# Kernel tuning notes

Measured on AMD Instinct MI355X. Metric: run time of the kernel, lower is better.

Reference implementation:

```python
import jax, jax.numpy as jnp
import numpy as np
import math

D_MODEL = 1024
N_HEADS = 16
HEAD_DIM = D_MODEL // N_HEADS
SEQ_LEN = 8192
INCLUDE_LOCAL = 2


def get_dilated_positions(seq_len, include_local=2):
    # Faithful numpy port of the torch pattern generator (runs once at setup).
    max_attend = include_local + int(math.ceil(math.log2(seq_len + 1)))
    positions = np.zeros((seq_len, max_attend), dtype=np.int64)
    mask = np.zeros((seq_len, max_attend), dtype=bool)
    for i in range(seq_len):
        ap = [i]
        for j in range(1, include_local + 1):
            if i - j >= 0:
                ap.append(i - j)
        k = 2
        while i - 2 ** k >= 0:
            ap.append(i - 2 ** k)
            k += 1
        positions[i, :len(ap)] = ap
        mask[i, :len(ap)] = True
    return positions, mask


def setup_inputs() -> dict:
    key = jax.random.key(0)
    kx, kq, kk, kv, ko = jax.random.split(key, 5)
    x = jax.random.normal(kx, (1, SEQ_LEN, D_MODEL), dtype=jnp.float32)
    # nn.Linear(bias=False) weights, torch layout [out_features, in_features]
    s = 0.02
    q_w = jax.random.normal(kq, (D_MODEL, D_MODEL), dtype=jnp.float32) * s
    k_w = jax.random.normal(kk, (D_MODEL, D_MODEL), dtype=jnp.float32) * s
    v_w = jax.random.normal(kv, (D_MODEL, D_MODEL), dtype=jnp.float32) * s
    o_w = jax.random.normal(ko, (D_MODEL, D_MODEL), dtype=jnp.float32) * s
    pos_np, mask_np = get_dilated_positions(SEQ_LEN, INCLUDE_LOCAL)
    return {
        "x": x,
        "q_w": q_w, "k_w": k_w, "v_w": v_w, "o_w": o_w,
        "positions": jnp.asarray(pos_np),   # (S, A) int64 indices
        "attend_mask": jnp.asarray(mask_np) # (S, A) bool
    }


def reference(x, q_w, k_w, v_w, o_w, positions, attend_mask):
    B, S, _ = x.shape
    H, Dh = N_HEADS, HEAD_DIM
    scale = Dh ** -0.5

    q = (x @ q_w.T).reshape(B, S, H, Dh).transpose(0, 2, 1, 3)  # (B,H,S,Dh)
    k = (x @ k_w.T).reshape(B, S, H, Dh).transpose(0, 2, 1, 3)
    v = (x @ v_w.T).reshape(B, S, H, Dh).transpose(0, 2, 1, 3)

    # Gather K/V at the dilated positions: (B,H,S,A,Dh)
    k_sparse = k[:, :, positions, :]
    v_sparse = v[:, :, positions, :]

    scores = jnp.einsum('bhsd,bhsad->bhsa', q, k_sparse) * scale
    scores = jnp.where(attend_mask[None, None, :, :], scores, -jnp.inf)
    attn = jax.nn.softmax(scores, axis=-1)  # dropout p in eval / 0.0 -> identity

    out = jnp.einsum('bhsa,bhsad->bhsd', attn, v_sparse)
    out = out.transpose(0, 2, 1, 3).reshape(B, S, D_MODEL)
    return out @ o_w.T
```

## Files before the change

### kernel.cpp

```cpp
#include <hip/hip_runtime.h>
#include <hip/hip_bf16.h>

typedef __bf16 bf16_t;
typedef __bf16 bf16x4 __attribute__((ext_vector_type(4)));
typedef __bf16 bf16x8 __attribute__((ext_vector_type(8)));
typedef float floatx16 __attribute__((ext_vector_type(16)));

#define SEQ    8192
#define DM     1024
#define NHEADS 16
#define HDIM   64

__device__ __forceinline__ void async_ld16(bf16_t* lds, const bf16_t* g) {
  __builtin_amdgcn_global_load_lds(
      (__attribute__((address_space(1))) void*)g,
      (__attribute__((address_space(3))) void*)lds, 16, 0, 0);
}

__global__ __launch_bounds__(256)
void cvt_all(const float* __restrict__ x,  const float* __restrict__ qw,
             const float* __restrict__ kw, const float* __restrict__ vw,
             const float* __restrict__ ow,
             bf16_t* __restrict__ Xb,  bf16_t* __restrict__ QWb,
             bf16_t* __restrict__ KWb, bf16_t* __restrict__ VWb,
             bf16_t* __restrict__ OWb) {
  const int b = blockIdx.x;
  const float* in; bf16_t* out; int g;
  if (b < 8192) { in = x; out = Xb; g = b; }
  else {
    const int w  = (b - 8192) >> 10;
    const int wb = (b - 8192) & 1023;
    switch (w) {
      case 0:  in = qw; out = QWb; break;
      case 1:  in = kw; out = KWb; break;
      case 2:  in = vw; out = VWb; break;
      default: in = ow; out = OWb; break;
    }
    g = wb;
  }
  const int idx = (g * 256 + threadIdx.x) * 4;
  float4 v = *(const float4*)(in + idx);
  bf16x4 o = { (bf16_t)v.x, (bf16_t)v.y, (bf16_t)v.z, (bf16_t)v.w };
  *(bf16x4*)(out + idx) = o;
}

__global__ __launch_bounds__(256)
void gemm_qkv(const bf16_t* __restrict__ A,
              const bf16_t* __restrict__ Bq, const bf16_t* __restrict__ Bk,
              const bf16_t* __restrict__ Bv,
              bf16_t* __restrict__ Cq, bf16_t* __restrict__ Ck, bf16_t* __restrict__ Cv)
{
  const bf16_t* B = (blockIdx.z == 0) ? Bq : (blockIdx.z == 1) ? Bk : Bv;
  bf16_t*       C = (blockIdx.z == 0) ? Cq : (blockIdx.z == 1) ? Ck : Cv;
  constexpr int Kdim = DM;
  __shared__ __attribute__((aligned(16))) bf16_t sA[128 * 64];
  __shared__ __attribute__((aligned(16))) bf16_t sB[128 * 64];

  const int tid  = threadIdx.x;
  const int wave = tid >> 6;
  const int lane = tid & 63;
  const int l31  = lane & 31;
  const int half = lane >> 5;
  const int wr   = (wave >> 1) * 64;
  const int wc   = (wave & 1) * 64;

  const int gc = (lane & 7) ^ ((lane >> 3) & 7);
  const size_t arow0 = (size_t)blockIdx.x * 128 + wave * 32 + (lane >> 3);
  const size_t brow0 = (size_t)blockIdx.y * 128 + wave * 32 + (lane >> 3);
  const bf16_t* Ag = A + arow0 * Kdim + gc * 8;
  const bf16_t* Bg = B + brow0 * Kdim + gc * 8;
  bf16_t* sAw = sA + wave * 32 * 64;
  bf16_t* sBw = sB + wave * 32 * 64;

  floatx16 acc[2][2];
  #pragma unroll
  for (int i = 0; i < 2; ++i)
    #pragma unroll
    for (int j = 0; j < 2; ++j)
      acc[i][j] = (floatx16)(0.0f);

  const int sw = l31 & 7;

  for (int ko = 0; ko < Kdim; ko += 64) {
    #pragma unroll
    for (int n = 0; n < 4; ++n) {
      async_ld16(sAw + n * 512, Ag + (size_t)n * 8 * Kdim + ko);
      async_ld16(sBw + n * 512, Bg + (size_t)n * 8 * Kdim + ko);
    }
    __syncthreads();

    #pragma unroll
    for (int s = 0; s < 4; ++s) {
      const int ck   = s * 2 + half;
      const int slot = (ck ^ sw) * 8;
      bf16x8 af[2], bfr[2];
      #pragma unroll
      for (int mi = 0; mi < 2; ++mi)
        af[mi] = *(const bf16x8*)&sA[(wr + mi * 32 + l31) * 64 + slot];
      #pragma unroll
      for (int ni = 0; ni < 2; ++ni)
        bfr[ni] = *(const bf16x8*)&sB[(wc + ni * 32 + l31) * 64 + slot];

      #pragma unroll
      for (int mi = 0; mi < 2; ++mi)
        #pragma unroll
        for (int ni = 0; ni < 2; ++ni)
          acc[mi][ni] = __builtin_amdgcn_mfma_f32_32x32x16_bf16(af[mi], bfr[ni], acc[mi][ni], 0, 0, 0);
    }

    __syncthreads();
  }

  const float scl = (blockIdx.z == 0) ? 0.125f : 1.0f;
  const int crow0 = blockIdx.x * 128 + wr + 4 * half;
  const int ccol0 = blockIdx.y * 128 + wc + l31;
  #pragma unroll
  for (int mi = 0; mi < 2; ++mi)
    #pragma unroll
    for (int ni = 0; ni < 2; ++ni)
      #pragma unroll
      for (int r = 0; r < 16; ++r) {
        const int row = crow0 + mi * 32 + (r & 3) + 8 * (r >> 2);
        C[(size_t)row * DM + (ccol0 + ni * 32)] = (bf16_t)(acc[mi][ni][r] * scl);
      }
}

__global__ __launch_bounds__(256)
void gemm_out(const bf16_t* __restrict__ A, const bf16_t* __restrict__ B,
              float* __restrict__ C)
{
  constexpr int Kdim = DM;
  __shared__ __attribute__((aligned(16))) bf16_t sA[128 * 32];
  __shared__ __attribute__((aligned(16))) bf16_t sB[64 * 32];

  const int tid  = threadIdx.x;
  const int wave = tid >> 6;
  const int lane = tid & 63;
  const int l31  = lane & 31;
  const int half = lane >> 5;
  const int wr   = (wave >> 1) * 64;
  const int wc   = (wave & 1) * 32;

  const int gc = (lane & 3) ^ ((lane >> 3) & 3);
  const size_t arow = (size_t)blockIdx.x * 128 + wave * 32 + (lane >> 2);
  const size_t brow = (size_t)blockIdx.y * 64 + wave * 16 + (lane >> 2);
  const bf16_t* Ag = A + arow * Kdim + gc * 8;
  const bf16_t* Bg = B + brow * Kdim + gc * 8;
  bf16_t* sAw = sA + wave * 32 * 32;
  bf16_t* sBw = sB + wave * 16 * 32;

  floatx16 acc[2];
  acc[0] = (floatx16)(0.0f);
  acc[1] = (floatx16)(0.0f);

  const int sw = (l31 >> 1) & 3;

  for (int ko = 0; ko < Kdim; ko += 32) {
    async_ld16(sAw,           Ag + ko);
    async_ld16(sAw + 16 * 32, Ag + 16 * Kdim + ko);
    async_ld16(sBw,           Bg + ko);
    __syncthreads();

    #pragma unroll
    for (int s = 0; s < 2; ++s) {
      const int ck   = s * 2 + half;
      const int slot = (ck ^ sw) * 8;
      bf16x8 af[2], bfr;
      #pragma unroll
      for (int mi = 0; mi < 2; ++mi)
        af[mi] = *(const bf16x8*)&sA[(wr + mi * 32 + l31) * 32 + slot];
      bfr = *(const bf16x8*)&sB[(wc + l31) * 32 + slot];

      #pragma unroll
      for (int mi = 0; mi < 2; ++mi)
        acc[mi] = __builtin_amdgcn_mfma_f32_32x32x16_bf16(af[mi], bfr, acc[mi], 0, 0, 0);
    }

    __syncthreads();
  }

  const int crow0 = blockIdx.x * 128 + wr + 4 * half;
  const int ccol  = blockIdx.y * 64 + wc + l31;
  #pragma unroll
  for (int mi = 0; mi < 2; ++mi)
    #pragma unroll
    for (int r = 0; r < 16; ++r) {
      const int row = crow0 + mi * 32 + (r & 3) + 8 * (r >> 2);
      C[(size_t)row * DM + ccol] = acc[mi][r];
    }
}

__global__ __launch_bounds__(256)
void dilated_attn(const bf16_t* __restrict__ Q, const bf16_t* __restrict__ K,
                  const bf16_t* __restrict__ V, bf16_t* O)
{
  __shared__ float sM[2][64];
  __shared__ float sL[2][64];
  __shared__ float sAcc[2][64][17];

  const int lane = threadIdx.x & 63;
  const int wv   = threadIdx.x >> 6;
  const int ql   = wv >> 1;
  const int sub  = wv & 1;
  const int qb   = (blockIdx.x & 7) * 512 + (blockIdx.x >> 3);
  const int i    = qb * 2 + ql;
  const size_t base = (size_t)i * DM + lane * 16;

  bf16x8 q0 = *(const bf16x8*)(Q + base);
  bf16x8 q1 = *(const bf16x8*)(Q + base + 8);
  float qf[16];
  #pragma unroll
  for (int j = 0; j < 8; ++j) { qf[j] = (float)q0[j]; qf[j + 8] = (float)q1[j]; }

  const int npos = (i == 0) ? 1 : (33 - __builtin_clz((unsigned)i));
  auto pos_addr = [&](int t) -> size_t {
    const int off = (t == 0) ? 0 : (1 << (t - 1));
    return (size_t)(i - off) * DM + lane * 16;
  };

  float m = -INFINITY, l = 0.0f;
  float acc[16];
  #pragma unroll
  for (int j = 0; j < 16; ++j) acc[j] = 0.0f;

  int t = sub;
  if (t < npos) {
    size_t a = pos_addr(t);
    bf16x8 k0 = *(const bf16x8*)(K + a), k1 = *(const bf16x8*)(K + a + 8);
    bf16x8 v0 = *(const bf16x8*)(V + a), v1 = *(const bf16x8*)(V + a + 8);
    while (true) {
      const int tn = t + 2;
      const bool more = (tn < npos);
      bf16x8 nk0, nk1, nv0, nv1;
      if (more) {
        const size_t na = pos_addr(tn);
        nk0 = *(const bf16x8*)(K + na); nk1 = *(const bf16x8*)(K + na + 8);
        nv0 = *(const bf16x8*)(V + na); nv1 = *(const bf16x8*)(V + na + 8);
      }

      float sc = 0.0f;
      #pragma unroll
      for (int j = 0; j < 8; ++j) sc += qf[j] * (float)k0[j] + qf[j + 8] * (float)k1[j];
      sc += __shfl_xor(sc, 1, 64);
      sc += __shfl_xor(sc, 2, 64);

      float mn = fmaxf(m, sc);
      float co = __expf(m - mn);
      float w  = __expf(sc - mn);
      l = l * co + w;
      m = mn;
      #pragma unroll
      for (int j = 0; j < 8; ++j) {
        acc[j]     = acc[j]     * co + w * (float)v0[j];
        acc[j + 8] = acc[j + 8] * co + w * (float)v1[j];
      }

      if (!more) break;
      k0 = nk0; k1 = nk1; v0 = nv0; v1 = nv1;
      t = tn;
    }
  }

  if (sub == 1) {
    sM[ql][lane] = m;
    sL[ql][lane] = l;
    #pragma unroll
    for (int j = 0; j < 16; ++j) sAcc[ql][lane][j] = acc[j];
  }
  __syncthreads();
  if (sub == 0) {
    const float mb = sM[ql][lane], lb = sL[ql][lane];
    const float mt = fmaxf(m, mb);
    const float ca = __expf(m - mt);
    const float cb = __expf(mb - mt);
    const float inv = 1.0f / (l * ca + lb * cb);
    bf16x8 o0, o1;
    #pragma unroll
    for (int j = 0; j < 8; ++j) {
      o0[j] = (bf16_t)((acc[j]     * ca + sAcc[ql][lane][j]     * cb) * inv);
      o1[j] = (bf16_t)((acc[j + 8] * ca + sAcc[ql][lane][j + 8] * cb) * inv);
    }
    *(bf16x8*)(O + base)     = o0;
    *(bf16x8*)(O + base + 8) = o1;
  }
}

extern "C" void kernel_launch(void* const* d_in, const int* in_sizes, int n_in,
                              void* d_out, int out_size, void* d_ws, size_t ws_size,
                              hipStream_t stream) {
  (void)in_sizes; (void)n_in; (void)out_size; (void)ws_size;
  const float* x  = (const float*)d_in[0];
  const float* qw = (const float*)d_in[1];
  const float* kw = (const float*)d_in[2];
  const float* vw = (const float*)d_in[3];
  const float* ow = (const float*)d_in[4];
  float* out = (float*)d_out;

  bf16_t* Xb  = (bf16_t*)d_ws;
  bf16_t* Qb  = Xb  + (size_t)SEQ * DM;
  bf16_t* Kb  = Qb  + (size_t)SEQ * DM;
  bf16_t* Vb  = Kb  + (size_t)SEQ * DM;
  bf16_t* QWb = Vb  + (size_t)SEQ * DM;
  bf16_t* KWb = QWb + (size_t)DM * DM;
  bf16_t* VWb = KWb + (size_t)DM * DM;
  bf16_t* OWb = VWb + (size_t)DM * DM;
  bf16_t* AO  = Qb;

  cvt_all<<<dim3(8192 + 4096), dim3(256), 0, stream>>>(x, qw, kw, vw, ow,
                                                       Xb, QWb, KWb, VWb, OWb);

  dim3 block(256);
  gemm_qkv<<<dim3(SEQ / 128, DM / 128, 3), block, 0, stream>>>(Xb, QWb, KWb, VWb, Qb, Kb, Vb);
  dilated_attn<<<dim3(SEQ / 2), block, 0, stream>>>(Qb, Kb, Vb, AO);
  gemm_out<<<dim3(SEQ / 128, DM / 64), block, 0, stream>>>(AO, OWb, out);
}
```

Before: 215.9 us.

## Unify GEMMs into double-buffered 256x128 tile core with 8 waves

Replaces the QKV and output GEMMs with one shared templated core that uses 256x128 tiles, 512 threads (8 waves) and double-buffered LDS. Global-to-LDS async loads for the next K tile are spread across the MFMA substeps, with barriers and raised wave priority around the MFMA groups. The goal is to hide load latency, overlap memory with compute, and cut per-tile barrier overhead and block count. In exchange it uses more LDS per block (96 KB), which may limit occupancy, and the output GEMM now launches fewer, larger blocks.

```diff
diff --git a/kernel.cpp b/kernel.cpp
--- a/kernel.cpp
+++ b/kernel.cpp
@@ -44,33 +44,29 @@
   *(bf16x4*)(out + idx) = o;
 }
 
-__global__ __launch_bounds__(256)
-void gemm_qkv(const bf16_t* __restrict__ A,
-              const bf16_t* __restrict__ Bq, const bf16_t* __restrict__ Bk,
-              const bf16_t* __restrict__ Bv,
-              bf16_t* __restrict__ Cq, bf16_t* __restrict__ Ck, bf16_t* __restrict__ Cv)
-{
-  const bf16_t* B = (blockIdx.z == 0) ? Bq : (blockIdx.z == 1) ? Bk : Bv;
-  bf16_t*       C = (blockIdx.z == 0) ? Cq : (blockIdx.z == 1) ? Ck : Cv;
+template <typename OutT>
+__device__ __forceinline__ void gemm_core_256x128(
+    const bf16_t* __restrict__ A, const bf16_t* __restrict__ B,
+    OutT* __restrict__ C, float scl)
+{
   constexpr int Kdim = DM;
-  __shared__ __attribute__((aligned(16))) bf16_t sA[128 * 64];
-  __shared__ __attribute__((aligned(16))) bf16_t sB[128 * 64];
+  constexpr int NT   = Kdim / 64;
+  __shared__ __attribute__((aligned(16))) bf16_t sA[2][256 * 64];
+  __shared__ __attribute__((aligned(16))) bf16_t sB[2][128 * 64];
 
   const int tid  = threadIdx.x;
   const int wave = tid >> 6;
   const int lane = tid & 63;
   const int l31  = lane & 31;
   const int half = lane >> 5;
-  const int wr   = (wave >> 1) * 64;
-  const int wc   = (wave & 1) * 64;
+  const int wm   = wave >> 1;
+  const int wn   = wave & 1;
 
   const int gc = (lane & 7) ^ ((lane >> 3) & 7);
-  const size_t arow0 = (size_t)blockIdx.x * 128 + wave * 32 + (lane >> 3);
-  const size_t brow0 = (size_t)blockIdx.y * 128 + wave * 32 + (lane >> 3);
-  const bf16_t* Ag = A + arow0 * Kdim + gc * 8;
-  const bf16_t* Bg = B + brow0 * Kdim + gc * 8;
-  bf16_t* sAw = sA + wave * 32 * 64;
-  bf16_t* sBw = sB + wave * 32 * 64;
+  const size_t arow = (size_t)blockIdx.x * 256 + wave * 8 + (lane >> 3);
+  const size_t brow = (size_t)blockIdx.y * 128 + wave * 8 + (lane >> 3);
+  const bf16_t* Ag = A + arow * Kdim + gc * 8;
+  const bf16_t* Bg = B + brow * Kdim + gc * 8;
 
   floatx16 acc[2][2];
   #pragma unroll
@@ -79,41 +75,58 @@
     for (int j = 0; j < 2; ++j)
       acc[i][j] = (floatx16)(0.0f);
 
+  #pragma unroll
+  for (int j = 0; j < 4; ++j)
+    async_ld16(&sA[0][(j * 64 + wave * 8) * 64], Ag + (size_t)j * 64 * Kdim);
+  #pragma unroll
+  for (int j = 0; j < 2; ++j)
+    async_ld16(&sB[0][(j * 64 + wave * 8) * 64], Bg + (size_t)j * 64 * Kdim);
+  __syncthreads();
+
   const int sw = l31 & 7;
 
-  for (int ko = 0; ko < Kdim; ko += 64) {
-    #pragma unroll
-    for (int n = 0; n < 4; ++n) {
-      async_ld16(sAw + n * 512, Ag + (size_t)n * 8 * Kdim + ko);
-      async_ld16(sBw + n * 512, Bg + (size_t)n * 8 * Kdim + ko);
-    }
+  for (int kt = 0; kt < NT; ++kt) {
+    const int  cur = kt & 1;
+    const int  nxt = cur ^ 1;
+    const int  ko  = (kt + 1) * 64;
+    const bool pre = (kt + 1 < NT);
+
+    #pragma unroll
+    for (int s = 0; s < 4; ++s) {
+      const int slot = ((s * 2 + half) ^ sw) * 8;
+      bf16x8 af0 = *(const bf16x8*)&sA[cur][(wm * 64      + l31) * 64 + slot];
+      bf16x8 af1 = *(const bf16x8*)&sA[cur][(wm * 64 + 32 + l31) * 64 + slot];
+      bf16x8 bf0 = *(const bf16x8*)&sB[cur][(wn * 64      + l31) * 64 + slot];
+      bf16x8 bf1 = *(const bf16x8*)&sB[cur][(wn * 64 + 32 + l31) * 64 + slot];
+
+      if (pre) {
+        if (s == 0) {
+          async_ld16(&sA[nxt][(0 * 64 + wave * 8) * 64], Ag + (size_t)0 * 64 * Kdim + ko);
+          async_ld16(&sA[nxt][(1 * 64 + wave * 8) * 64], Ag + (size_t)1 * 64 * Kdim + ko);
+        } else if (s == 1) {
+          async_ld16(&sA[nxt][(2 * 64 + wave * 8) * 64], Ag + (size_t)2 * 64 * Kdim + ko);
+          async_ld16(&sA[nxt][(3 * 64 + wave * 8) * 64], Ag + (size_t)3 * 64 * Kdim + ko);
+        } else if (s == 2) {
+          async_ld16(&sB[nxt][(0 * 64 + wave * 8) * 64], Bg + ko);
+          async_ld16(&sB[nxt][(1 * 64 + wave * 8) * 64], Bg + (size_t)64 * Kdim + ko);
+        }
+      }
+
+      __builtin_amdgcn_s_barrier();
+      __builtin_amdgcn_s_setprio(1);
+      acc[0][0] = __builtin_amdgcn_mfma_f32_32x32x16_bf16(af0, bf0, acc[0][0], 0, 0, 0);
+      acc[0][1] = __builtin_amdgcn_mfma_f32_32x32x16_bf16(af0, bf1, acc[0][1], 0, 0, 0);
+      acc[1][0] = __builtin_amdgcn_mfma_f32_32x32x16_bf16(af1, bf0, acc[1][0], 0, 0, 0);
+      acc[1][1] = __builtin_amdgcn_mfma_f32_32x32x16_bf16(af1, bf1, acc[1][1], 0, 0, 0);
+      __builtin_amdgcn_s_setprio(0);
+      if (s < 3) __builtin_amdgcn_s_barrier();
+    }
+
     __syncthreads();
-
-    #pragma unroll
-    for (int s = 0; s < 4; ++s) {
-      const int ck   = s * 2 + half;
-      const int slot = (ck ^ sw) * 8;
-      bf16x8 af[2], bfr[2];
-      #pragma unroll
-      for (int mi = 0; mi < 2; ++mi)
-        af[mi] = *(const bf16x8*)&sA[(wr + mi * 32 + l31) * 64 + slot];
-      #pragma unroll
-      for (int ni = 0; ni < 2; ++ni)
-        bfr[ni] = *(const bf16x8*)&sB[(wc + ni * 32 + l31) * 64 + slot];
-
-      #pragma unroll
-      for (int mi = 0; mi < 2; ++mi)
-        #pragma unroll
-        for (int ni = 0; ni < 2; ++ni)
-          acc[mi][ni] = __builtin_amdgcn_mfma_f32_32x32x16_bf16(af[mi], bfr[ni], acc[mi][ni], 0, 0, 0);
-    }
-
-    __syncthreads();
-  }
-
-  const float scl = (blockIdx.z == 0) ? 0.125f : 1.0f;
-  const int crow0 = blockIdx.x * 128 + wr + 4 * half;
-  const int ccol0 = blockIdx.y * 128 + wc + l31;
+  }
+
+  const int crow0 = blockIdx.x * 256 + wm * 64 + 4 * half;
+  const int ccol0 = blockIdx.y * 128 + wn * 64 + l31;
   #pragma unroll
   for (int mi = 0; mi < 2; ++mi)
     #pragma unroll
@@ -121,73 +134,27 @@
       #pragma unroll
       for (int r = 0; r < 16; ++r) {
         const int row = crow0 + mi * 32 + (r & 3) + 8 * (r >> 2);
-        C[(size_t)row * DM + (ccol0 + ni * 32)] = (bf16_t)(acc[mi][ni][r] * scl);
-      }
-}
-
-__global__ __launch_bounds__(256)
+        C[(size_t)row * DM + (ccol0 + ni * 32)] = (OutT)(acc[mi][ni][r] * scl);
+      }
+}
+
+__global__ __launch_bounds__(512, 2)
+void gemm_qkv(const bf16_t* __restrict__ A,
+              const bf16_t* __restrict__ Bq, const bf16_t* __restrict__ Bk,
+              const bf16_t* __restrict__ Bv,
+              bf16_t* __restrict__ Cq, bf16_t* __restrict__ Ck, bf16_t* __restrict__ Cv)
+{
+  const bf16_t* B = (blockIdx.z == 0) ? Bq : (blockIdx.z == 1) ? Bk : Bv;
+  bf16_t*       C = (blockIdx.z == 0) ? Cq : (blockIdx.z == 1) ? Ck : Cv;
+  const float scl = (blockIdx.z == 0) ? 0.125f : 1.0f;
+  gemm_core_256x128<bf16_t>(A, B, C, scl);
+}
+
+__global__ __launch_bounds__(512, 2)
 void gemm_out(const bf16_t* __restrict__ A, const bf16_t* __restrict__ B,
               float* __restrict__ C)
 {
-  constexpr int Kdim = DM;
-  __shared__ __attribute__((aligned(16))) bf16_t sA[128 * 32];
-  __shared__ __attribute__((aligned(16))) bf16_t sB[64 * 32];
-
-  const int tid  = threadIdx.x;
-  const int wave = tid >> 6;
-  const int lane = tid & 63;
-  const int l31  = lane & 31;
-  const int half = lane >> 5;
-  const int wr   = (wave >> 1) * 64;
-  const int wc   = (wave & 1) * 32;
-
-  const int gc = (lane & 3) ^ ((lane >> 3) & 3);
-  const size_t arow = (size_t)blockIdx.x * 128 + wave * 32 + (lane >> 2);
-  const size_t brow = (size_t)blockIdx.y * 64 + wave * 16 + (lane >> 2);
-  const bf16_t* Ag = A + arow * Kdim + gc * 8;
-  const bf16_t* Bg = B + brow * Kdim + gc * 8;
-  bf16_t* sAw = sA + wave * 32 * 32;
-  bf16_t* sBw = sB + wave * 16 * 32;
-
-  floatx16 acc[2];
-  acc[0] = (floatx16)(0.0f);
-  acc[1] = (floatx16)(0.0f);
-
-  const int sw = (l31 >> 1) & 3;
-
-  for (int ko = 0; ko < Kdim; ko += 32) {
-    async_ld16(sAw,           Ag + ko);
-    async_ld16(sAw + 16 * 32, Ag + 16 * Kdim + ko);
-    async_ld16(sBw,           Bg + ko);
-    __syncthreads();
-
-    #pragma unroll
-    for (int s = 0; s < 2; ++s) {
-      const int ck   = s * 2 + half;
-      const int slot = (ck ^ sw) * 8;
-      bf16x8 af[2], bfr;
-      #pragma unroll
-      for (int mi = 0; mi < 2; ++mi)
-        af[mi] = *(const bf16x8*)&sA[(wr + mi * 32 + l31) * 32 + slot];
-      bfr = *(const bf16x8*)&sB[(wc + l31) * 32 + slot];
-
-      #pragma unroll
-      for (int mi = 0; mi < 2; ++mi)
-        acc[mi] = __builtin_amdgcn_mfma_f32_32x32x16_bf16(af[mi], bfr, acc[mi], 0, 0, 0);
-    }
-
-    __syncthreads();
-  }
-
-  const int crow0 = blockIdx.x * 128 + wr + 4 * half;
-  const int ccol  = blockIdx.y * 64 + wc + l31;
-  #pragma unroll
-  for (int mi = 0; mi < 2; ++mi)
-    #pragma unroll
-    for (int r = 0; r < 16; ++r) {
-      const int row = crow0 + mi * 32 + (r & 3) + 8 * (r >> 2);
-      C[(size_t)row * DM + ccol] = acc[mi][r];
-    }
+  gemm_core_256x128<float>(A, B, C, 1.0f);
 }
 
 __global__ __launch_bounds__(256)
@@ -309,8 +276,7 @@
   cvt_all<<<dim3(8192 + 4096), dim3(256), 0, stream>>>(x, qw, kw, vw, ow,
                                                        Xb, QWb, KWb, VWb, OWb);
 
-  dim3 block(256);
-  gemm_qkv<<<dim3(SEQ / 128, DM / 128, 3), block, 0, stream>>>(Xb, QWb, KWb, VWb, Qb, Kb, Vb);
-  dilated_attn<<<dim3(SEQ / 2), block, 0, stream>>>(Qb, Kb, Vb, AO);
-  gemm_out<<<dim3(SEQ / 128, DM / 64), block, 0, stream>>>(AO, OWb, out);
-}
+  gemm_qkv<<<dim3(SEQ / 256, DM / 128, 3), dim3(512), 0, stream>>>(Xb, QWb, KWb, VWb, Qb, Kb, Vb);
+  dilated_attn<<<dim3(SEQ / 2), dim3(256), 0, stream>>>(Qb, Kb, Vb, AO);
+  gemm_out<<<dim3(SEQ / 256, DM / 128), dim3(512), 0, stream>>>(AO, OWb, out);
+}
```

Result: slower. 224.2 us (+3.8%).
